# Performance work log

Hardware: AMD Instinct MI355X
Metric: run time of the kernel (lower is better)

The kernel has to match this reference:

```python
import jax, jax.numpy as jnp
import numpy as np

MD = 4                  # corr_md
D = 2 * MD + 1          # patch_size = 9


def setup_inputs() -> dict:
    key = jax.random.key(0)
    k1, k2 = jax.random.split(key)
    b, c, h, w = 4, 128, 128, 256
    t1 = jax.random.normal(k1, (b, c, h, w), dtype=jnp.float32)
    t2 = jax.random.normal(k2, (b, c, h, w), dtype=jnp.float32)
    return {"t1": t1, "t2": t2}


def reference(t1, t2):
    # Local cost volume: for each displacement (di, dj) in [-MD, MD]^2,
    # out[b, p, y, x] = sum_c t1[b, c, y, x] * t2[b, c, y+di, x+dj]
    # with zero padding outside t2 (SpatialCorrelationSampler semantics,
    # kernel_size=1, stride=1, dilation_patch=1; no channel normalization).
    b, c, h, w = t1.shape
    t2p = jnp.pad(t2, ((0, 0), (0, 0), (MD, MD), (MD, MD)))
    # Loop over the fixed 9x9 displacement grid (81 small reductions);
    outs = [
        jnp.einsum('bchw,bchw->bhw', t1, t2p[:, :, i:i + h, j:j + w])
        for i in range(D) for j in range(D)
    ]
    return jnp.stack(outs, axis=1)  # [b, 81, h, w]
```

## Files before the change

### kernel.cpp

```cpp
#include <hip/hip_runtime.h>

#define NP 81
#define CC 128
#define HH 128
#define WW 256

typedef __attribute__((ext_vector_type(8))) short short8;
typedef __attribute__((ext_vector_type(4))) float f32x4;
typedef __attribute__((ext_vector_type(16))) float f32x16;

__device__ __forceinline__ short f2bf(float f) {
    unsigned int u = __builtin_bit_cast(unsigned int, f);
    u += 0x7fffu + ((u >> 16) & 1u);
    return (short)(u >> 16);
}

__global__ __launch_bounds__(1024, 4) void corr_fused(
        const float* __restrict__ t1, const float* __restrict__ t2,
        float* __restrict__ out) {
    const int bid = blockIdx.x;
    const int sw  = (bid & 7) * 64 + (bid >> 3);
    const int xt    = sw & 7;
    const int strip = (sw >> 3) & 15;
    const int b     = sw >> 7;
    const int X0 = xt * 32;
    const int y0 = strip * 8;

    const int tid  = threadIdx.x;
    const int lane = tid & 63;
    const int w    = tid >> 6;
    const int n    = lane & 31;
    const int g    = lane >> 5;

    __shared__ short sA[8 * 32 * 128];
    __shared__ float obufs[16 * 9 * 36];

    const size_t plane = (size_t)HH * WW;
    const int r = y0 - 4 + w;

    short8 bre[8][2];
    {
        const bool rok = (r >= 0) && (r < HH);
#pragma unroll
        for (int t = 0; t < 2; ++t) {
            const int x2 = X0 - 4 + n + 32 * t;
            if (rok && x2 >= 0 && x2 < WW) {
                const float* p = t2 + ((size_t)(b * CC + g * 8) * HH + r) * WW + x2;
#pragma unroll
                for (int kc = 0; kc < 8; ++kc) {
                    short8 f;
#pragma unroll
                    for (int j = 0; j < 8; ++j)
                        f[j] = f2bf(p[(size_t)(kc * 16 + j) * plane]);
                    bre[kc][t] = f;
                }
            } else {
#pragma unroll
                for (int kc = 0; kc < 8; ++kc)
                    bre[kc][t] = (short8){0,0,0,0,0,0,0,0};
            }
        }
    }

#pragma unroll
    for (int i = 0; i < 4; ++i) {
        const int unit = tid + i * 1024;
        const int x   = unit & 31;
        const int oct = (unit >> 5) & 15;
        const int yy  = unit >> 9;
        const float* p = t1 + ((size_t)(b * CC + oct * 8) * HH + (y0 + yy)) * WW
                       + X0 + x;
        short8 pk;
#pragma unroll
        for (int j = 0; j < 8; ++j) pk[j] = f2bf(p[(size_t)j * plane]);
        *(short8*)&sA[yy * 4096 + x * 128 + ((oct ^ (x & 15)) * 8)] = pk;
    }
    __syncthreads();

    const int ylo = (w > 8) ? (w - 8) : 0;
    const int yhi = (w < 7) ? w : 7;
    float* ob = &obufs[w * 324];

    for (int yy = ylo; yy <= yhi; ++yy) {
        const int sbase = yy * 4096 + n * 128;

        f32x16 a0;
#pragma unroll
        for (int q = 0; q < 16; ++q) a0[q] = 0.f;
#pragma unroll
        for (int kc = 0; kc < 8; ++kc) {
            const short8 af = *(const short8*)
                &sA[sbase + (((kc * 2 + g) ^ (n & 15)) * 8)];
            a0 = __builtin_amdgcn_mfma_f32_32x32x16_bf16(af, bre[kc][0], a0, 0, 0, 0);
        }
#pragma unroll
        for (int q = 0; q < 16; ++q) {
            const int m  = (q & 3) + 8 * (q >> 2) + 4 * g;
            const int dj = n - m;
            if (dj >= 0 && dj <= 8) ob[dj * 36 + m] = a0[q];
        }

        f32x16 a1;
#pragma unroll
        for (int q = 0; q < 16; ++q) a1[q] = 0.f;
#pragma unroll
        for (int kc = 0; kc < 8; ++kc) {
            const short8 af = *(const short8*)
                &sA[sbase + (((kc * 2 + g) ^ (n & 15)) * 8)];
            a1 = __builtin_amdgcn_mfma_f32_32x32x16_bf16(af, bre[kc][1], a1, 0, 0, 0);
        }
#pragma unroll
        for (int q = 0; q < 16; ++q) {
            const int m  = (q & 3) + 8 * (q >> 2) + 4 * g;
            const int dj = n - m + 32;
            if (dj >= 0 && dj <= 8) ob[dj * 36 + m] = a1[q];
        }

        const int di = w - yy;
        const int y  = y0 + yy;
        float* obase = out + ((size_t)(b * NP + di * 9) * HH + y) * WW + X0;
#pragma unroll
        for (int k = 0; k < 2; ++k) {
            const int u = lane + k * 64;
            if (u < 72) {
                const int dj = u >> 3, xq = u & 7;
                f32x4 v = *(const f32x4*)&ob[dj * 36 + xq * 4];
                *(f32x4*)&obase[(size_t)dj * plane + xq * 4] = v;
            }
        }
    }
}

extern "C" void kernel_launch(void* const* d_in, const int* in_sizes, int n_in,
                              void* d_out, int out_size, void* d_ws, size_t ws_size,
                              hipStream_t stream) {
    const float* t1 = (const float*)d_in[0];
    const float* t2 = (const float*)d_in[1];
    corr_fused<<<512, 1024, 0, stream>>>(t1, t2, (float*)d_out);
}
```

Measured before the change: 224.8 us.

## Shrink x-tile to 24 columns so one MFMA covers tile plus halo

Reduces the per-block x tile from 32 to 24 output columns so that the 24 outputs plus an 8-column halo fit in a single 32-wide MFMA B operand. This halves the MFMA count, t2 register loads and register pressure per block, but grows the grid from 512 to 704 blocks and reloads more halo overall. The last x tile is partial and needs bounds guards, and the launch-bounds occupancy hint is dropped.

```diff
diff --git a/kernel.cpp b/kernel.cpp
--- a/kernel.cpp
+++ b/kernel.cpp
@@ -4,6 +4,9 @@
 #define CC 128
 #define HH 128
 #define WW 256
+#define SX 24
+#define NXT 11
+#define NBLK (NXT * 16 * 4)
 
 typedef __attribute__((ext_vector_type(8))) short short8;
 typedef __attribute__((ext_vector_type(4))) float f32x4;
@@ -15,16 +18,17 @@
     return (short)(u >> 16);
 }
 
-__global__ __launch_bounds__(1024, 4) void corr_fused(
+__global__ __launch_bounds__(1024) void corr_fused24(
         const float* __restrict__ t1, const float* __restrict__ t2,
         float* __restrict__ out) {
     const int bid = blockIdx.x;
-    const int sw  = (bid & 7) * 64 + (bid >> 3);
-    const int xt    = sw & 7;
-    const int strip = (sw >> 3) & 15;
-    const int b     = sw >> 7;
-    const int X0 = xt * 32;
-    const int y0 = strip * 8;
+    const int sw  = (bid & 7) * (NBLK / 8) + (bid >> 3);
+    const int ys = sw & 15;
+    const int v  = sw >> 4;
+    const int xt = v % NXT;
+    const int b  = v / NXT;
+    const int X0 = xt * SX;
+    const int y0 = ys * 8;
 
     const int tid  = threadIdx.x;
     const int lane = tid & 63;
@@ -32,100 +36,82 @@
     const int n    = lane & 31;
     const int g    = lane >> 5;
 
-    __shared__ short sA[8 * 32 * 128];
-    __shared__ float obufs[16 * 9 * 36];
+    __shared__ short sA[8 * SX * 128];
+    __shared__ __align__(16) float obufs[16 * 9 * 28];
 
     const size_t plane = (size_t)HH * WW;
     const int r = y0 - 4 + w;
 
-    short8 bre[8][2];
+    short8 bre[8];
     {
-        const bool rok = (r >= 0) && (r < HH);
+        const int x2 = X0 - 4 + n;
+        if (r >= 0 && r < HH && x2 >= 0 && x2 < WW) {
+            const float* p = t2 + ((size_t)(b * CC + g * 8) * HH + r) * WW + x2;
 #pragma unroll
-        for (int t = 0; t < 2; ++t) {
-            const int x2 = X0 - 4 + n + 32 * t;
-            if (rok && x2 >= 0 && x2 < WW) {
-                const float* p = t2 + ((size_t)(b * CC + g * 8) * HH + r) * WW + x2;
+            for (int kc = 0; kc < 8; ++kc) {
+                short8 f;
 #pragma unroll
-                for (int kc = 0; kc < 8; ++kc) {
-                    short8 f;
+                for (int j = 0; j < 8; ++j)
+                    f[j] = f2bf(p[(size_t)(kc * 16 + j) * plane]);
+                bre[kc] = f;
+            }
+        } else {
 #pragma unroll
-                    for (int j = 0; j < 8; ++j)
-                        f[j] = f2bf(p[(size_t)(kc * 16 + j) * plane]);
-                    bre[kc][t] = f;
-                }
-            } else {
-#pragma unroll
-                for (int kc = 0; kc < 8; ++kc)
-                    bre[kc][t] = (short8){0,0,0,0,0,0,0,0};
-            }
+            for (int kc = 0; kc < 8; ++kc)
+                bre[kc] = (short8){0,0,0,0,0,0,0,0};
         }
     }
 
 #pragma unroll
-    for (int i = 0; i < 4; ++i) {
+    for (int i = 0; i < 3; ++i) {
         const int unit = tid + i * 1024;
-        const int x   = unit & 31;
-        const int oct = (unit >> 5) & 15;
-        const int yy  = unit >> 9;
-        const float* p = t1 + ((size_t)(b * CC + oct * 8) * HH + (y0 + yy)) * WW
-                       + X0 + x;
-        short8 pk;
+        const int x    = unit % SX;
+        const int rest = unit / SX;
+        const int oct  = rest & 15;
+        const int yy   = rest >> 4;
+        short8 pk = {0,0,0,0,0,0,0,0};
+        if (X0 + x < WW) {
+            const float* p = t1 + ((size_t)(b * CC + oct * 8) * HH + (y0 + yy)) * WW
+                           + X0 + x;
 #pragma unroll
-        for (int j = 0; j < 8; ++j) pk[j] = f2bf(p[(size_t)j * plane]);
-        *(short8*)&sA[yy * 4096 + x * 128 + ((oct ^ (x & 15)) * 8)] = pk;
+            for (int j = 0; j < 8; ++j) pk[j] = f2bf(p[(size_t)j * plane]);
+        }
+        *(short8*)&sA[yy * (SX * 128) + x * 128 + ((oct ^ (x & 15)) * 8)] = pk;
     }
     __syncthreads();
 
     const int ylo = (w > 8) ? (w - 8) : 0;
     const int yhi = (w < 7) ? w : 7;
-    float* ob = &obufs[w * 324];
+    float* ob = &obufs[w * 252];
 
     for (int yy = ylo; yy <= yhi; ++yy) {
-        const int sbase = yy * 4096 + n * 128;
+        const int sbase = yy * (SX * 128) + n * 128;
 
-        f32x16 a0;
+        f32x16 a;
 #pragma unroll
-        for (int q = 0; q < 16; ++q) a0[q] = 0.f;
+        for (int q = 0; q < 16; ++q) a[q] = 0.f;
 #pragma unroll
         for (int kc = 0; kc < 8; ++kc) {
             const short8 af = *(const short8*)
                 &sA[sbase + (((kc * 2 + g) ^ (n & 15)) * 8)];
-            a0 = __builtin_amdgcn_mfma_f32_32x32x16_bf16(af, bre[kc][0], a0, 0, 0, 0);
+            a = __builtin_amdgcn_mfma_f32_32x32x16_bf16(af, bre[kc], a, 0, 0, 0);
         }
+
 #pragma unroll
         for (int q = 0; q < 16; ++q) {
             const int m  = (q & 3) + 8 * (q >> 2) + 4 * g;
             const int dj = n - m;
-            if (dj >= 0 && dj <= 8) ob[dj * 36 + m] = a0[q];
-        }
-
-        f32x16 a1;
-#pragma unroll
-        for (int q = 0; q < 16; ++q) a1[q] = 0.f;
-#pragma unroll
-        for (int kc = 0; kc < 8; ++kc) {
-            const short8 af = *(const short8*)
-                &sA[sbase + (((kc * 2 + g) ^ (n & 15)) * 8)];
-            a1 = __builtin_amdgcn_mfma_f32_32x32x16_bf16(af, bre[kc][1], a1, 0, 0, 0);
-        }
-#pragma unroll
-        for (int q = 0; q < 16; ++q) {
-            const int m  = (q & 3) + 8 * (q >> 2) + 4 * g;
-            const int dj = n - m + 32;
-            if (dj >= 0 && dj <= 8) ob[dj * 36 + m] = a1[q];
+            if (dj >= 0 && dj <= 8 && m < SX) ob[dj * 28 + m] = a[q];
         }
 
         const int di = w - yy;
         const int y  = y0 + yy;
-        float* obase = out + ((size_t)(b * NP + di * 9) * HH + y) * WW + X0;
-#pragma unroll
-        for (int k = 0; k < 2; ++k) {
-            const int u = lane + k * 64;
-            if (u < 72) {
-                const int dj = u >> 3, xq = u & 7;
-                f32x4 v = *(const f32x4*)&ob[dj * 36 + xq * 4];
-                *(f32x4*)&obase[(size_t)dj * plane + xq * 4] = v;
+        if (lane < 54) {
+            const int dj = lane / 6, xq = lane % 6;
+            if (X0 + xq * 4 < WW) {
+                f32x4 vv = *(const f32x4*)&ob[dj * 28 + xq * 4];
+                *(f32x4*)&out[((size_t)(b * NP + di * 9 + dj) * HH + y) * WW
+                              + X0 + xq * 4] = vv;
             }
         }
     }
@@ -136,5 +122,5 @@
                               hipStream_t stream) {
     const float* t1 = (const float*)d_in[0];
     const float* t2 = (const float*)d_in[1];
-    corr_fused<<<512, 1024, 0, stream>>>(t1, t2, (float*)d_out);
+    corr_fused24<<<NBLK, 1024, 0, stream>>>(t1, t2, (float*)d_out);
 }
```

After: 190.5 us. 15.2% less time.
